# Kernel optimization log

Measured on AMD Instinct MI355X. Metric: run time of the kernel, lower is better.

## Reference

```python
import jax, jax.numpy as jnp
import numpy as np

VOCAB, D, A, NEG = 32000, 200, 20, 2
NUM_USERS, NUM_ITEMS = 100000, 50000
R, L, B, NNZ = 4096, 128, 1024, 20480
EPS = 1e-12

def _norm(x, axis):
    n = jnp.sqrt(jnp.sum(x * x, axis=axis, keepdims=True))
    return x / jnp.maximum(n, EPS)

def setup_inputs() -> dict:
    key = jax.random.key(0)
    ks = jax.random.split(key, 20)
    rows_u = jax.random.randint(ks[5], (NNZ,), 0, B)
    cols_u = jax.random.randint(ks[6], (NNZ,), 0, R)
    rows_i = jax.random.randint(ks[7], (NNZ,), 0, B)
    cols_i = jax.random.randint(ks[8], (NNZ,), 0, R)
    return {
        "historical_review": jax.random.randint(ks[0], (R, L), 0, VOCAB),
        "neg_review": jax.random.randint(ks[1], (R * NEG, L), 0, VOCAB),
        "user": jax.random.randint(ks[2], (B,), 0, NUM_USERS),
        "item": jax.random.randint(ks[3], (B,), 0, NUM_ITEMS),
        "label": jax.random.uniform(ks[4], (B,), jnp.float32, 1.0, 5.0),
        "user_histor_index": jnp.stack([rows_u, cols_u]),
        "user_histor_value": jax.random.uniform(ks[9], (NNZ,), jnp.float32),
        "item_histor_index": jnp.stack([rows_i, cols_i]),
        "item_histor_value": jax.random.uniform(ks[10], (NNZ,), jnp.float32),
        "word_emb": jax.random.normal(ks[11], (VOCAB, D), jnp.float32),
        "Wm": jax.random.normal(ks[12], (D, D), jnp.float32) * 0.05,
        "Ww": jax.random.normal(ks[13], (A, D), jnp.float32) * 0.05,
        "bw": jnp.zeros((A,), jnp.float32),
        "Wt": jax.random.normal(ks[14], (D, A), jnp.float32) * 0.05,
        "fc_w": jax.random.uniform(ks[15], (1, 2 * D), jnp.float32, -0.05, 0.05),
        "fc_b": jnp.zeros((1,), jnp.float32),
        "fm_V": jax.random.uniform(ks[16], (2 * D, 10), jnp.float32, -0.05, 0.05),
        "b_users": jax.random.uniform(ks[17], (NUM_USERS, 1), jnp.float32, 0.0, 0.1),
        "b_items": jax.random.uniform(ks[18], (NUM_ITEMS, 1), jnp.float32, 0.0, 0.1),
    }

def reference(historical_review, neg_review, user, item, label,
              user_histor_index, user_histor_value,
              item_histor_index, item_histor_value,
              word_emb, Wm, Ww, bw, Wt, fc_w, fc_b, fm_V, b_users, b_items):
    # ABAE attention over each review
    e_w = word_emb[historical_review]              # (R, L, D)
    y_s = jnp.mean(e_w, axis=1)                    # (R, D)
    z_n = jnp.mean(word_emb[neg_review], axis=1)   # (R*NEG, D)
    dx = jnp.einsum('rld,rd->rl', e_w @ Wm.T, y_s) # (R, L)
    ax = jax.nn.softmax(dx, axis=1)
    # Faithful to source: view(R, D, L) is a raw reshape, not a transpose.
    z_s = jnp.einsum('rdl,rl->rd', e_w.reshape(R, D, L), ax)  # (R, D)
    p_t = z_s @ Ww.T + bw                          # (R, A)
    r_s = p_t @ Wt.T                               # (R, D)
    # cosine margin ranking loss
    c1 = jnp.sum(_norm(r_s, 1) * _norm(z_s, 1), axis=-1)      # (R,)
    c1 = jnp.repeat(c1, NEG)                                   # (R*NEG,)
    c2 = jnp.sum(_norm(z_n.reshape(R, NEG, D), 2) * _norm(r_s, 1)[:, None, :], axis=-1).reshape(-1)
    abae_out_loss = jax.nn.relu(c2 - c1 + 1.0)     # margin=1, target=+1
    J_loss = jnp.mean(abae_out_loss)
    # aspect-matrix orthogonality regularizer
    Tn = _norm(Wt, 0)                              # normalize columns (dim=0)
    U_loss = jnp.mean((Tn.T @ Tn - jnp.eye(A, dtype=Wt.dtype)) ** 2)
    # sparse (B, R) @ (R, D) aggregation via segment_sum
    user_aspect_embed = jax.ops.segment_sum(
        user_histor_value[:, None] * r_s[user_histor_index[1]],
        user_histor_index[0], num_segments=B)      # (B, D)
    item_aspect_embed = jax.ops.segment_sum(
        item_histor_value[:, None] * r_s[item_histor_index[1]],
        item_histor_index[0], num_segments=B)      # (B, D)
    input_vec = jnp.concatenate([user_aspect_embed, item_aspect_embed], axis=1)  # (B, 2D)
    fm_linear = input_vec @ fc_w.T + fc_b          # (B, 1)
    fm_i1 = (input_vec @ fm_V) ** 2
    fm_i2 = (input_vec ** 2) @ (fm_V ** 2)
    # NOTE: faithful to source, the quadratic term is summed over the whole batch (scalar)
    fm_output = 0.5 * jnp.sum(fm_i1 - fm_i2) + fm_linear + b_users[user] + b_items[item]
    prediction = fm_output.squeeze(1)              # (B,)
    rating_loss = (prediction - label) ** 2
    mse_loss = jnp.mean(rating_loss)
    obj_loss = mse_loss + 0.01 * J_loss + 0.01 * U_loss
    return (obj_loss, rating_loss, abae_out_loss, prediction, user_aspect_embed, item_aspect_embed)
```

## Files before the change

kernel.cpp:

```cpp
#include <hip/hip_runtime.h>
#include <hip/hip_fp16.h>
#include <math.h>

#define R_TOT 4096
#define L_LEN 128
#define D_DIM 200
#define A_DIM 20
#define NEGK  2
#define B_SZ  1024
#define NNZ_C 20480
#define RN_TOT (R_TOT*NEGK)
#define S_TOT (R_TOT + RN_TOT)
#define VOCAB_C 32000
#define EPS_ 1e-12f
#define SLOT_CAP 64
#define NBUCK_BLK 160

__device__ __forceinline__ float4 unpack4(const uint2 u) {
  union { unsigned v; __half2 h; } c0, c1;
  c0.v = u.x; c1.v = u.y;
  const float2 f0 = __half22float2(c0.h);
  const float2 f1 = __half22float2(c1.h);
  return make_float4(f0.x, f0.y, f1.x, f1.y);
}

__global__ __launch_bounds__(256) void k_cast(
    const float* __restrict__ emb, ushort* __restrict__ emb_h, int* __restrict__ cnt)
{
  if (blockIdx.x == 0) {
    for (int i = threadIdx.x; i < 2*B_SZ; i += 256) cnt[i] = 0;
  }
  const int idx = blockIdx.x*256 + threadIdx.x;
  if (idx < (VOCAB_C*D_DIM)/4) {
    const float4 v = reinterpret_cast<const float4*>(emb)[idx];
    ushort4 o;
    o.x = __half_as_ushort(__float2half(v.x));
    o.y = __half_as_ushort(__float2half(v.y));
    o.z = __half_as_ushort(__float2half(v.z));
    o.w = __half_as_ushort(__float2half(v.w));
    reinterpret_cast<ushort4*>(emb_h)[idx] = o;
  }
}

#define ACC8(Q) { \
  const float4 e0_ = unpack4(make_uint2((Q).x,(Q).y)); \
  const float4 e1_ = unpack4(make_uint2((Q).z,(Q).w)); \
  sA.x+=e0_.x; sA.y+=e0_.y; sA.z+=e0_.z; sA.w+=e0_.w; \
  sB.x+=e1_.x; sB.y+=e1_.y; sB.z+=e1_.z; sB.w+=e1_.w; }

__global__ __launch_bounds__(256, 8) void k_means2(
    const int* __restrict__ hist, const int* __restrict__ neg,
    const ushort* __restrict__ emb_h,
    float* __restrict__ ys_all, float* __restrict__ zn_all,
    const int* __restrict__ uidx, const float* __restrict__ uval,
    const int* __restrict__ iidx, const float* __restrict__ ival,
    int* __restrict__ cnt, int* __restrict__ scol, float* __restrict__ sval)
{
  const int sb = blockIdx.x;
  const int tid = threadIdx.x;

  if (sb >= S_TOT) {
    const int g = (sb - S_TOT)*256 + tid;
    if (g < NNZ_C) {
      const int b = uidx[g];
      const int slot = atomicAdd(&cnt[b], 1);
      if (slot < SLOT_CAP) {
        scol[b*SLOT_CAP + slot] = uidx[NNZ_C + g];
        sval[b*SLOT_CAP + slot] = uval[g];
      }
    } else {
      const int g2 = g - NNZ_C;
      const int b = iidx[g2];
      const int slot = atomicAdd(&cnt[B_SZ + b], 1);
      if (slot < SLOT_CAP) {
        scol[(B_SZ + b)*SLOT_CAP + slot] = iidx[NNZ_C + g2];
        sval[(B_SZ + b)*SLOT_CAP + slot] = ival[g2];
      }
    }
    return;
  }

  __shared__ int widx[L_LEN];
  __shared__ __align__(16) float part[8][D_DIM];
  const bool is_pos = (sb < R_TOT);
  const int* src = is_pos ? (hist + (size_t)sb*L_LEN)
                          : (neg + (size_t)(sb - R_TOT)*L_LEN);
  if (tid < L_LEN) widx[tid] = src[tid];
  __syncthreads();

  const int c5 = tid & 31;
  const int j  = tid >> 5;
  float4 sA = {0.f,0.f,0.f,0.f}, sB = {0.f,0.f,0.f,0.f};
  if (c5 < 25) {
    const size_t coff = 8*c5;
    uint4 q0 = *reinterpret_cast<const uint4*>(emb_h + (size_t)widx[j +   0]*D_DIM + coff);
    uint4 q1 = *reinterpret_cast<const uint4*>(emb_h + (size_t)widx[j +   8]*D_DIM + coff);
    uint4 q2 = *reinterpret_cast<const uint4*>(emb_h + (size_t)widx[j +  16]*D_DIM + coff);
    uint4 q3 = *reinterpret_cast<const uint4*>(emb_h + (size_t)widx[j +  24]*D_DIM + coff);
    uint4 q4 = *reinterpret_cast<const uint4*>(emb_h + (size_t)widx[j +  32]*D_DIM + coff);
    uint4 q5 = *reinterpret_cast<const uint4*>(emb_h + (size_t)widx[j +  40]*D_DIM + coff);
    uint4 q6 = *reinterpret_cast<const uint4*>(emb_h + (size_t)widx[j +  48]*D_DIM + coff);
    uint4 q7 = *reinterpret_cast<const uint4*>(emb_h + (size_t)widx[j +  56]*D_DIM + coff);
    ACC8(q0) ACC8(q1) ACC8(q2) ACC8(q3) ACC8(q4) ACC8(q5) ACC8(q6) ACC8(q7)
    q0 = *reinterpret_cast<const uint4*>(emb_h + (size_t)widx[j +  64]*D_DIM + coff);
    q1 = *reinterpret_cast<const uint4*>(emb_h + (size_t)widx[j +  72]*D_DIM + coff);
    q2 = *reinterpret_cast<const uint4*>(emb_h + (size_t)widx[j +  80]*D_DIM + coff);
    q3 = *reinterpret_cast<const uint4*>(emb_h + (size_t)widx[j +  88]*D_DIM + coff);
    q4 = *reinterpret_cast<const uint4*>(emb_h + (size_t)widx[j +  96]*D_DIM + coff);
    q5 = *reinterpret_cast<const uint4*>(emb_h + (size_t)widx[j + 104]*D_DIM + coff);
    q6 = *reinterpret_cast<const uint4*>(emb_h + (size_t)widx[j + 112]*D_DIM + coff);
    q7 = *reinterpret_cast<const uint4*>(emb_h + (size_t)widx[j + 120]*D_DIM + coff);
    ACC8(q0) ACC8(q1) ACC8(q2) ACC8(q3) ACC8(q4) ACC8(q5) ACC8(q6) ACC8(q7)
    *reinterpret_cast<float4*>(&part[j][8*c5])     = sA;
    *reinterpret_cast<float4*>(&part[j][8*c5 + 4]) = sB;
  }
  __syncthreads();
  float* dst = is_pos ? (ys_all + (size_t)sb*D_DIM)
                      : (zn_all + (size_t)(sb - R_TOT)*D_DIM);
  if (tid < D_DIM) {
    float a = 0.f;
    #pragma unroll
    for (int j2 = 0; j2 < 8; ++j2) a += part[j2][tid];
    dst[tid] = a * (1.0f/128.0f);
  }
}

#define KB_RT 16
__global__ __launch_bounds__(256, 2) void k_matvec(
    const float* __restrict__ ys_all, const float* __restrict__ Wm,
    float* __restrict__ vv_all)
{
  __shared__ float ysl[KB_RT][D_DIM];
  const int r0 = blockIdx.x * KB_RT;
  const int tid = threadIdx.x;
  for (int i = tid; i < KB_RT*D_DIM; i += 256)
    ysl[i / D_DIM][i % D_DIM] = ys_all[(size_t)r0*D_DIM + i];
  __syncthreads();
  if (tid < D_DIM) {
    float acc[KB_RT];
    #pragma unroll
    for (int r = 0; r < KB_RT; ++r) acc[r] = 0.f;
    #pragma unroll 4
    for (int k = 0; k < D_DIM; ++k) {
      const float w = Wm[k*D_DIM + tid];
      #pragma unroll
      for (int r = 0; r < KB_RT; ++r) acc[r] += ysl[r][k] * w;
    }
    #pragma unroll
    for (int r = 0; r < KB_RT; ++r)
      vv_all[(size_t)(r0 + r)*D_DIM + tid] = acc[r];
  }
}

__global__ __launch_bounds__(512, 4) void k_attn(
    const int* __restrict__ hist, const ushort* __restrict__ emb_h,
    const float* __restrict__ vv_all,
    const float* __restrict__ Ww, const float* __restrict__ bw,
    const float* __restrict__ Wt, const float* __restrict__ zn_all,
    float* __restrict__ rs_out, float* __restrict__ abae)
{
  __shared__ __align__(16) ushort ew[L_LEN*D_DIM];
  __shared__ __align__(16) float ax[L_LEN];
  __shared__ __align__(16) float zs[D_DIM];
  __shared__ __align__(16) float ubuf[240];
  int*   widx  = reinterpret_cast<int*>(ubuf);
  float* ptile = ubuf;
  float* red   = ubuf + 160;

  const int r = blockIdx.x;
  const int tid = threadIdx.x, lane = tid & 63, wv = tid >> 6;
  const int c5 = tid & 31;
  const int j  = tid >> 5;
  const bool act = (c5 < 25);
  const int coff = 8*c5;

  if (tid < L_LEN) widx[tid] = hist[r*L_LEN + tid];
  float4 v8a = {0,0,0,0}, v8b = {0,0,0,0};
  if (act) {
    v8a = *reinterpret_cast<const float4*>(vv_all + (size_t)r*D_DIM + coff);
    v8b = *reinterpret_cast<const float4*>(vv_all + (size_t)r*D_DIM + coff + 4);
  }
  __syncthreads();

  float zn0 = 0.f, zn1 = 0.f;
  float p0=0.f,p1=0.f,p2=0.f,p3=0.f,p4=0.f,p5=0.f,p6=0.f,p7=0.f;
  {
    uint4 q0,q1,q2,q3,q4,q5,q6,q7;
    if (act) {
      q0 = *reinterpret_cast<const uint4*>(emb_h + (size_t)widx[j +   0]*D_DIM + coff);
      q1 = *reinterpret_cast<const uint4*>(emb_h + (size_t)widx[j +  16]*D_DIM + coff);
      q2 = *reinterpret_cast<const uint4*>(emb_h + (size_t)widx[j +  32]*D_DIM + coff);
      q3 = *reinterpret_cast<const uint4*>(emb_h + (size_t)widx[j +  48]*D_DIM + coff);
      q4 = *reinterpret_cast<const uint4*>(emb_h + (size_t)widx[j +  64]*D_DIM + coff);
      q5 = *reinterpret_cast<const uint4*>(emb_h + (size_t)widx[j +  80]*D_DIM + coff);
      q6 = *reinterpret_cast<const uint4*>(emb_h + (size_t)widx[j +  96]*D_DIM + coff);
      q7 = *reinterpret_cast<const uint4*>(emb_h + (size_t)widx[j + 112]*D_DIM + coff);
    }
    if (tid < D_DIM) {
      zn0 = zn_all[(size_t)(2*r)*D_DIM + tid];
      zn1 = zn_all[(size_t)(2*r + 1)*D_DIM + tid];
    }
    if (act) {
      #define STG(K, Q, P) { \
        *reinterpret_cast<uint4*>(ew + (j + 16*(K))*D_DIM + coff) = Q; \
        const float4 e0_ = unpack4(make_uint2(Q.x, Q.y)); \
        const float4 e1_ = unpack4(make_uint2(Q.z, Q.w)); \
        P = e0_.x*v8a.x + e0_.y*v8a.y + e0_.z*v8a.z + e0_.w*v8a.w \
          + e1_.x*v8b.x + e1_.y*v8b.y + e1_.z*v8b.z + e1_.w*v8b.w; }
      STG(0,q0,p0) STG(1,q1,p1) STG(2,q2,p2) STG(3,q3,p3)
      STG(4,q4,p4) STG(5,q5,p5) STG(6,q6,p6) STG(7,q7,p7)
      #undef STG
    }
  }
  #pragma unroll
  for (int o = 16; o > 0; o >>= 1) {
    p0 += __shfl_xor(p0, o); p1 += __shfl_xor(p1, o);
    p2 += __shfl_xor(p2, o); p3 += __shfl_xor(p3, o);
    p4 += __shfl_xor(p4, o); p5 += __shfl_xor(p5, o);
    p6 += __shfl_xor(p6, o); p7 += __shfl_xor(p7, o);
  }
  if (c5 == 0) {
    ax[j]      = p0; ax[j + 16]  = p1; ax[j + 32]  = p2; ax[j + 48]  = p3;
    ax[j + 64] = p4; ax[j + 80]  = p5; ax[j + 96]  = p6; ax[j + 112] = p7;
  }
  __syncthreads();

  if (tid < 64) {
    float m = fmaxf(ax[tid], ax[tid+64]);
    #pragma unroll
    for (int o = 32; o > 0; o >>= 1) m = fmaxf(m, __shfl_xor(m, o));
    if (tid == 0) red[0] = m;
  }
  __syncthreads();
  const float M = red[0];
  if (tid < L_LEN) {
    float e = expf(ax[tid] - M);
    ax[tid] = e;
    float s = e;
    #pragma unroll
    for (int o = 32; o > 0; o >>= 1) s += __shfl_xor(s, o);
    if (lane == 0) red[1 + wv] = s;
  }
  __syncthreads();

  {
    const float Sinv = 1.0f / (red[1] + red[2]);
    const int lq = lane & 15;
    const int quad = lane >> 4;
    const float4 ax8a = *reinterpret_cast<const float4*>(ax + 8*lq);
    const float4 ax8b = *reinterpret_cast<const float4*>(ax + 8*lq + 4);
    for (int dq = wv; dq < 50; dq += 8) {
      const int d0 = 4*dq + quad;
      const int f0 = (d0 << 7) + 8*lq;
      const uint4 q = *reinterpret_cast<const uint4*>(ew + f0);
      const float4 e0 = unpack4(make_uint2(q.x, q.y));
      const float4 e1 = unpack4(make_uint2(q.z, q.w));
      float a = e0.x*ax8a.x + e0.y*ax8a.y + e0.z*ax8a.z + e0.w*ax8a.w
              + e1.x*ax8b.x + e1.y*ax8b.y + e1.z*ax8b.z + e1.w*ax8b.w;
      #pragma unroll
      for (int o = 8; o > 0; o >>= 1) a += __shfl_xor(a, o);
      if (lq == 0) zs[d0] = a * Sinv;
    }
  }
  __syncthreads();

  if (tid < 160) {
    const int a = tid % 20, jj = tid / 20;
    float s = 0.f;
    #pragma unroll
    for (int ii = 0; ii < 25; ++ii) {
      const int d = jj + 8*ii;
      s += zs[d] * Ww[a*D_DIM + d];
    }
    ptile[tid] = s;
  }
  __syncthreads();
  if (tid < A_DIM) {
    float s = bw[tid];
    #pragma unroll
    for (int jj = 0; jj < 8; ++jj) s += ptile[jj*20 + tid];
    red[2 + tid] = s;
  }
  __syncthreads();

  float rsd = 0.f, zsd = 0.f;
  if (tid < D_DIM) {
    float acc = 0.f;
    #pragma unroll
    for (int a = 0; a < A_DIM; ++a) acc += red[2+a] * Wt[tid*A_DIM + a];
    rsd = acc; zsd = zs[tid];
    rs_out[(size_t)r*D_DIM + tid] = acc;
  } else { zn0 = 0.f; zn1 = 0.f; }
  float a0 = rsd*rsd, a1 = zsd*zsd, a2 = rsd*zsd;
  float b0 = zn0*zn0, b1 = zn0*rsd, b2 = zn1*zn1, b3 = zn1*rsd;
  #pragma unroll
  for (int o = 32; o > 0; o >>= 1) {
    a0 += __shfl_xor(a0, o); a1 += __shfl_xor(a1, o); a2 += __shfl_xor(a2, o);
    b0 += __shfl_xor(b0, o); b1 += __shfl_xor(b1, o);
    b2 += __shfl_xor(b2, o); b3 += __shfl_xor(b3, o);
  }
  if (lane == 0) {
    red[22 + 0*8 + wv] = a0; red[22 + 1*8 + wv] = a1; red[22 + 2*8 + wv] = a2;
    red[22 + 3*8 + wv] = b0; red[22 + 4*8 + wv] = b1;
    red[22 + 5*8 + wv] = b2; red[22 + 6*8 + wv] = b3;
  }
  __syncthreads();

  if (tid < 64) {
    const int qi = tid >> 3, k = tid & 7;
    float v = (qi < 7) ? red[22 + 8*qi + k] : 0.f;
    v += __shfl_xor(v, 1); v += __shfl_xor(v, 2); v += __shfl_xor(v, 4);
    const float s0 = __shfl(v, 0),  s1 = __shfl(v, 8),  s2 = __shfl(v, 16);
    const float t0 = __shfl(v, 24), t1 = __shfl(v, 32);
    const float t2 = __shfl(v, 40), t3 = __shfl(v, 48);
    if (tid == 0) {
      const float nr = fmaxf(sqrtf(s0), EPS_);
      const float nz = fmaxf(sqrtf(s1), EPS_);
      const float c1 = s2 / (nr * nz);
      const float c2a = t1 / (fmaxf(sqrtf(t0), EPS_) * nr);
      const float c2b = t3 / (fmaxf(sqrtf(t2), EPS_) * nr);
      abae[2*r]     = fmaxf(c2a - c1 + 1.0f, 0.0f);
      abae[2*r + 1] = fmaxf(c2b - c1 + 1.0f, 0.0f);
    }
  }
}

__global__ __launch_bounds__(512) void k_aggfm(
    const int* __restrict__ cnt, const int* __restrict__ scol,
    const float* __restrict__ sval, const float* __restrict__ rs,
    const float* __restrict__ fcw, const float* __restrict__ V,
    float* __restrict__ uae, float* __restrict__ iae,
    float* __restrict__ linb, float* __restrict__ quadb)
{
  __shared__ __align__(16) float ivec[2*D_DIM];
  __shared__ float redw[8];
  __shared__ float qpart[10];
  const int b = blockIdx.x;
  const int tid = threadIdx.x, lane = tid & 63, wv = tid >> 6;

  if (tid < D_DIM) {
    int n = cnt[b]; n = n < SLOT_CAP ? n : SLOT_CAP;
    const int* cols = scol + (size_t)b*SLOT_CAP;
    const float* vals = sval + (size_t)b*SLOT_CAP;
    float acc = 0.f;
    for (int j = 0; j < n; ++j) acc += vals[j] * rs[(size_t)cols[j]*D_DIM + tid];
    ivec[tid] = acc;
    uae[(size_t)b*D_DIM + tid] = acc;
  } else if (tid >= 256 && tid < 256 + D_DIM) {
    const int t = tid - 256;
    int n = cnt[B_SZ + b]; n = n < SLOT_CAP ? n : SLOT_CAP;
    const int* cols = scol + (size_t)(B_SZ + b)*SLOT_CAP;
    const float* vals = sval + (size_t)(B_SZ + b)*SLOT_CAP;
    float acc = 0.f;
    for (int j = 0; j < n; ++j) acc += vals[j] * rs[(size_t)cols[j]*D_DIM + t];
    ivec[D_DIM + t] = acc;
    iae[(size_t)b*D_DIM + t] = acc;
  }
  __syncthreads();

  float lv = 0.f;
  if (tid < 2*D_DIM) lv = ivec[tid] * fcw[tid];
  #pragma unroll
  for (int o = 32; o > 0; o >>= 1) lv += __shfl_xor(lv, o);
  if (lane == 0) redw[wv] = lv;

  {
    const int k = wv;
    float s1 = 0.f, s2 = 0.f;
    for (int f = lane; f < 2*D_DIM; f += 64) {
      const float x = ivec[f];
      const float vk = V[f*10 + k];
      s1 += x*vk; s2 += x*x*vk*vk;
    }
    #pragma unroll
    for (int o = 32; o > 0; o >>= 1) { s1 += __shfl_xor(s1,o); s2 += __shfl_xor(s2,o); }
    if (lane == 0) qpart[k] = s1*s1 - s2;
  }
  if (wv < 2) {
    const int k = 8 + wv;
    float s1 = 0.f, s2 = 0.f;
    for (int f = lane; f < 2*D_DIM; f += 64) {
      const float x = ivec[f];
      const float vk = V[f*10 + k];
      s1 += x*vk; s2 += x*x*vk*vk;
    }
    #pragma unroll
    for (int o = 32; o > 0; o >>= 1) { s1 += __shfl_xor(s1,o); s2 += __shfl_xor(s2,o); }
    if (lane == 0) qpart[k] = s1*s1 - s2;
  }
  __syncthreads();
  if (tid == 0) {
    float lin = 0.f;
    #pragma unroll
    for (int i = 0; i < 8; ++i) lin += redw[i];
    float q = 0.f;
    #pragma unroll
    for (int i = 0; i < 10; ++i) q += qpart[i];
    linb[b] = lin; quadb[b] = q;
  }
}

__global__ __launch_bounds__(1024) void k_final2(
    const float* __restrict__ quadb, const float* __restrict__ linb,
    const float* __restrict__ fcb, const int* __restrict__ user,
    const int* __restrict__ item, const float* __restrict__ busers,
    const float* __restrict__ bitems, const float* __restrict__ label,
    const float* __restrict__ Wt, const float* __restrict__ abae,
    float* __restrict__ pred, float* __restrict__ rl, float* __restrict__ obj)
{
  __shared__ float sA[16], sB[16], sC[16];
  __shared__ float cninv[A_DIM];
  __shared__ float quad_s;
  const int tid = threadIdx.x;
  const int lane = tid & 63;
  const int wv = tid >> 6;

  float q = quadb[tid];
  #pragma unroll
  for (int o = 32; o > 0; o >>= 1) q += __shfl_xor(q, o);
  if (lane == 0) sA[wv] = q;

  if (tid < A_DIM) {
    float s = 0.f;
    for (int d = 0; d < D_DIM; ++d) { const float w = Wt[d*A_DIM + tid]; s += w*w; }
    cninv[tid] = 1.0f / fmaxf(sqrtf(s), EPS_);
  }
  __syncthreads();
  if (wv == 0) {
    float s = (lane < 16) ? sA[lane] : 0.f;
    #pragma unroll
    for (int o = 32; o > 0; o >>= 1) s += __shfl_xor(s, o);
    if (lane == 0) quad_s = s;
  }
  __syncthreads();

  const float p = 0.5f*quad_s + linb[tid] + fcb[0]
                + busers[user[tid]] + bitems[item[tid]];
  pred[tid] = p;
  const float dd = p - label[tid];
  const float myrl = dd*dd;
  rl[tid] = myrl;

  float u = 0.f;
  if (tid < 400) {
    const int a = tid / 20, c = tid % 20;
    float dot = 0.f;
    for (int d = 0; d < D_DIM; ++d) dot += Wt[d*A_DIM + a]*Wt[d*A_DIM + c];
    const float g = dot*cninv[a]*cninv[c] - (a==c ? 1.0f : 0.0f);
    u = g*g;
  }
  float js = 0.f;
  #pragma unroll
  for (int j = 0; j < 8; ++j) js += abae[tid + 1024*j];
  float ms = myrl;

  #pragma unroll
  for (int o = 32; o > 0; o >>= 1) {
    u += __shfl_xor(u,o); js += __shfl_xor(js,o); ms += __shfl_xor(ms,o);
  }
  if (lane == 0) { sA[wv] = u; sB[wv] = js; sC[wv] = ms; }
  __syncthreads();
  if (tid == 0) {
    float U = 0.f, J = 0.f, Ms = 0.f;
    for (int i = 0; i < 16; ++i) { U += sA[i]; J += sB[i]; Ms += sC[i]; }
    obj[0] = Ms/1024.0f + 0.01f*(J/8192.0f) + 0.01f*(U/400.0f);
  }
}

extern "C" void kernel_launch(void* const* d_in, const int* in_sizes, int n_in,
                              void* d_out, int out_size, void* d_ws, size_t ws_size,
                              hipStream_t stream) {
  const int*   hist   = (const int*)  d_in[0];
  const int*   neg    = (const int*)  d_in[1];
  const int*   user   = (const int*)  d_in[2];
  const int*   item   = (const int*)  d_in[3];
  const float* label  = (const float*)d_in[4];
  const int*   uidx   = (const int*)  d_in[5];
  const float* uval   = (const float*)d_in[6];
  const int*   iidx   = (const int*)  d_in[7];
  const float* ival   = (const float*)d_in[8];
  const float* emb    = (const float*)d_in[9];
  const float* Wm     = (const float*)d_in[10];
  const float* Ww     = (const float*)d_in[11];
  const float* bw     = (const float*)d_in[12];
  const float* Wt     = (const float*)d_in[13];
  const float* fcw    = (const float*)d_in[14];
  const float* fcb    = (const float*)d_in[15];
  const float* V      = (const float*)d_in[16];
  const float* busers = (const float*)d_in[17];
  const float* bitems = (const float*)d_in[18];

  float* out  = (float*)d_out;
  float* obj  = out;
  float* rl   = out + 1;
  float* abae = out + 1 + B_SZ;
  float* pred = out + 1 + B_SZ + RN_TOT;
  float* uae  = pred + B_SZ;
  float* iae  = uae + (size_t)B_SZ*D_DIM;

  float* ws     = (float*)d_ws;
  float* rs     = ws;
  float* ys_all = rs + (size_t)R_TOT*D_DIM;
  float* zn_all = ys_all + (size_t)R_TOT*D_DIM;
  float* vv_all = zn_all + (size_t)RN_TOT*D_DIM;
  float* linb   = vv_all + (size_t)R_TOT*D_DIM;
  float* quadb  = linb + B_SZ;
  float* sval   = quadb + B_SZ;
  int*   scol   = (int*)(sval + (size_t)2*B_SZ*SLOT_CAP);
  int*   cnt    = scol + (size_t)2*B_SZ*SLOT_CAP;
  ushort* emb_h = (ushort*)(cnt + 2*B_SZ);

  const int cast_blocks = (VOCAB_C*D_DIM/4 + 255)/256;

  k_cast  <<<cast_blocks, 256, 0, stream>>>(emb, emb_h, cnt);
  k_means2<<<S_TOT + NBUCK_BLK, 256, 0, stream>>>(hist, neg, emb_h,
                                                  ys_all, zn_all,
                                                  uidx, uval, iidx, ival,
                                                  cnt, scol, sval);
  k_matvec<<<R_TOT/KB_RT, 256, 0, stream>>>(ys_all, Wm, vv_all);
  k_attn  <<<R_TOT, 512, 0, stream>>>(hist, emb_h, vv_all, Ww, bw, Wt,
                                      zn_all, rs, abae);
  k_aggfm <<<B_SZ, 512, 0, stream>>>(cnt, scol, sval, rs, fcw, V,
                                     uae, iae, linb, quadb);
  k_final2<<<1, 1024, 0, stream>>>(quadb, linb, fcb, user, item, busers, bitems,
                                   label, Wt, abae, pred, rl, obj);
}
```

Measured before the change: 309.2 us.

## Keep gathered embeddings in registers, reduce with DPP, raise attn occupancy

```diff
diff --git a/kernel.cpp b/kernel.cpp
--- a/kernel.cpp
+++ b/kernel.cpp
@@ -22,6 +22,39 @@
   const float2 f0 = __half22float2(c0.h);
   const float2 f1 = __half22float2(c1.h);
   return make_float4(f0.x, f0.y, f1.x, f1.y);
+}
+
+__device__ __forceinline__ float dot8h(const uint4 q, const float4 va, const float4 vb) {
+  const float4 e0 = unpack4(make_uint2(q.x, q.y));
+  const float4 e1 = unpack4(make_uint2(q.z, q.w));
+  return e0.x*va.x + e0.y*va.y + e0.z*va.z + e0.w*va.w
+       + e1.x*vb.x + e1.y*vb.y + e1.z*vb.z + e1.w*vb.w;
+}
+
+#define DPPI(old_, src_, ctrl, rmask) \
+  __builtin_amdgcn_update_dpp(old_, src_, ctrl, rmask, 0xf, false)
+
+__device__ __forceinline__ float dpp_sum32(float s) {
+  s += __int_as_float(DPPI(0, __float_as_int(s), 0x111, 0xf));
+  s += __int_as_float(DPPI(0, __float_as_int(s), 0x112, 0xf));
+  s += __int_as_float(DPPI(0, __float_as_int(s), 0x114, 0xf));
+  s += __int_as_float(DPPI(0, __float_as_int(s), 0x118, 0xf));
+  s += __int_as_float(DPPI(0, __float_as_int(s), 0x142, 0xa));
+  return s;
+}
+__device__ __forceinline__ float dpp_sum64(float s) {
+  s = dpp_sum32(s);
+  s += __int_as_float(DPPI(0, __float_as_int(s), 0x143, 0xc));
+  return s;
+}
+__device__ __forceinline__ float dpp_max64(float s) {
+  s = fmaxf(s, __int_as_float(DPPI(__float_as_int(s), __float_as_int(s), 0x111, 0xf)));
+  s = fmaxf(s, __int_as_float(DPPI(__float_as_int(s), __float_as_int(s), 0x112, 0xf)));
+  s = fmaxf(s, __int_as_float(DPPI(__float_as_int(s), __float_as_int(s), 0x114, 0xf)));
+  s = fmaxf(s, __int_as_float(DPPI(__float_as_int(s), __float_as_int(s), 0x118, 0xf)));
+  s = fmaxf(s, __int_as_float(DPPI(__float_as_int(s), __float_as_int(s), 0x142, 0xa)));
+  s = fmaxf(s, __int_as_float(DPPI(__float_as_int(s), __float_as_int(s), 0x143, 0xc)));
+  return s;
 }
 
 __global__ __launch_bounds__(256) void k_cast(
@@ -152,14 +185,14 @@
   }
 }
 
-__global__ __launch_bounds__(512, 4) void k_attn(
+__global__ __launch_bounds__(512, 6) void k_attn(
     const int* __restrict__ hist, const ushort* __restrict__ emb_h,
     const float* __restrict__ vv_all,
     const float* __restrict__ Ww, const float* __restrict__ bw,
     const float* __restrict__ Wt, const float* __restrict__ zn_all,
     float* __restrict__ rs_out, float* __restrict__ abae)
 {
-  __shared__ __align__(16) ushort ew[L_LEN*D_DIM];
+  __shared__ __align__(16) float part[D_DIM][16];
   __shared__ __align__(16) float ax[L_LEN];
   __shared__ __align__(16) float zs[D_DIM];
   __shared__ __align__(16) float ubuf[240];
@@ -182,85 +215,79 @@
   }
   __syncthreads();
 
+  uint4 q0,q1,q2,q3,q4,q5,q6,q7;
+  q0=q1=q2=q3=q4=q5=q6=q7=make_uint4(0,0,0,0);
   float zn0 = 0.f, zn1 = 0.f;
   float p0=0.f,p1=0.f,p2=0.f,p3=0.f,p4=0.f,p5=0.f,p6=0.f,p7=0.f;
-  {
-    uint4 q0,q1,q2,q3,q4,q5,q6,q7;
-    if (act) {
-      q0 = *reinterpret_cast<const uint4*>(emb_h + (size_t)widx[j +   0]*D_DIM + coff);
-      q1 = *reinterpret_cast<const uint4*>(emb_h + (size_t)widx[j +  16]*D_DIM + coff);
-      q2 = *reinterpret_cast<const uint4*>(emb_h + (size_t)widx[j +  32]*D_DIM + coff);
-      q3 = *reinterpret_cast<const uint4*>(emb_h + (size_t)widx[j +  48]*D_DIM + coff);
-      q4 = *reinterpret_cast<const uint4*>(emb_h + (size_t)widx[j +  64]*D_DIM + coff);
-      q5 = *reinterpret_cast<const uint4*>(emb_h + (size_t)widx[j +  80]*D_DIM + coff);
-      q6 = *reinterpret_cast<const uint4*>(emb_h + (size_t)widx[j +  96]*D_DIM + coff);
-      q7 = *reinterpret_cast<const uint4*>(emb_h + (size_t)widx[j + 112]*D_DIM + coff);
-    }
-    if (tid < D_DIM) {
-      zn0 = zn_all[(size_t)(2*r)*D_DIM + tid];
-      zn1 = zn_all[(size_t)(2*r + 1)*D_DIM + tid];
-    }
-    if (act) {
-      #define STG(K, Q, P) { \
-        *reinterpret_cast<uint4*>(ew + (j + 16*(K))*D_DIM + coff) = Q; \
-        const float4 e0_ = unpack4(make_uint2(Q.x, Q.y)); \
-        const float4 e1_ = unpack4(make_uint2(Q.z, Q.w)); \
-        P = e0_.x*v8a.x + e0_.y*v8a.y + e0_.z*v8a.z + e0_.w*v8a.w \
-          + e1_.x*v8b.x + e1_.y*v8b.y + e1_.z*v8b.z + e1_.w*v8b.w; }
-      STG(0,q0,p0) STG(1,q1,p1) STG(2,q2,p2) STG(3,q3,p3)
-      STG(4,q4,p4) STG(5,q5,p5) STG(6,q6,p6) STG(7,q7,p7)
-      #undef STG
-    }
-  }
-  #pragma unroll
-  for (int o = 16; o > 0; o >>= 1) {
-    p0 += __shfl_xor(p0, o); p1 += __shfl_xor(p1, o);
-    p2 += __shfl_xor(p2, o); p3 += __shfl_xor(p3, o);
-    p4 += __shfl_xor(p4, o); p5 += __shfl_xor(p5, o);
-    p6 += __shfl_xor(p6, o); p7 += __shfl_xor(p7, o);
-  }
-  if (c5 == 0) {
+  if (act) {
+    q0 = *reinterpret_cast<const uint4*>(emb_h + (size_t)widx[j +   0]*D_DIM + coff);
+    q1 = *reinterpret_cast<const uint4*>(emb_h + (size_t)widx[j +  16]*D_DIM + coff);
+    q2 = *reinterpret_cast<const uint4*>(emb_h + (size_t)widx[j +  32]*D_DIM + coff);
+    q3 = *reinterpret_cast<const uint4*>(emb_h + (size_t)widx[j +  48]*D_DIM + coff);
+    q4 = *reinterpret_cast<const uint4*>(emb_h + (size_t)widx[j +  64]*D_DIM + coff);
+    q5 = *reinterpret_cast<const uint4*>(emb_h + (size_t)widx[j +  80]*D_DIM + coff);
+    q6 = *reinterpret_cast<const uint4*>(emb_h + (size_t)widx[j +  96]*D_DIM + coff);
+    q7 = *reinterpret_cast<const uint4*>(emb_h + (size_t)widx[j + 112]*D_DIM + coff);
+  }
+  if (tid < D_DIM) {
+    zn0 = zn_all[(size_t)(2*r)*D_DIM + tid];
+    zn1 = zn_all[(size_t)(2*r + 1)*D_DIM + tid];
+  }
+  if (act) {
+    p0 = dot8h(q0, v8a, v8b); p1 = dot8h(q1, v8a, v8b);
+    p2 = dot8h(q2, v8a, v8b); p3 = dot8h(q3, v8a, v8b);
+    p4 = dot8h(q4, v8a, v8b); p5 = dot8h(q5, v8a, v8b);
+    p6 = dot8h(q6, v8a, v8b); p7 = dot8h(q7, v8a, v8b);
+  }
+  p0 = dpp_sum32(p0); p1 = dpp_sum32(p1); p2 = dpp_sum32(p2); p3 = dpp_sum32(p3);
+  p4 = dpp_sum32(p4); p5 = dpp_sum32(p5); p6 = dpp_sum32(p6); p7 = dpp_sum32(p7);
+  if (c5 == 31) {
     ax[j]      = p0; ax[j + 16]  = p1; ax[j + 32]  = p2; ax[j + 48]  = p3;
     ax[j + 64] = p4; ax[j + 80]  = p5; ax[j + 96]  = p6; ax[j + 112] = p7;
   }
   __syncthreads();
 
   if (tid < 64) {
-    float m = fmaxf(ax[tid], ax[tid+64]);
-    #pragma unroll
-    for (int o = 32; o > 0; o >>= 1) m = fmaxf(m, __shfl_xor(m, o));
-    if (tid == 0) red[0] = m;
+    float m = dpp_max64(fmaxf(ax[tid], ax[tid+64]));
+    if (tid == 63) red[0] = m;
   }
   __syncthreads();
   const float M = red[0];
   if (tid < L_LEN) {
-    float e = expf(ax[tid] - M);
+    const float e = expf(ax[tid] - M);
     ax[tid] = e;
-    float s = e;
-    #pragma unroll
-    for (int o = 32; o > 0; o >>= 1) s += __shfl_xor(s, o);
-    if (lane == 0) red[1 + wv] = s;
-  }
-  __syncthreads();
-
-  {
+    const float s = dpp_sum64(e);
+    if (lane == 63) red[1 + wv] = s;
+  }
+  __syncthreads();
+
+  if (act) {
+    const int Y  = 25*j + c5;
+    const int l0 = (8*Y) & 127;
+    const int v0 = Y >> 4;
+    const int sl = Y & 15;
+    const float4 ax8a = *reinterpret_cast<const float4*>(ax + l0);
+    const float4 ax8b = *reinterpret_cast<const float4*>(ax + l0 + 4);
+    part[v0 +   0][sl] = dot8h(q0, ax8a, ax8b);
+    part[v0 +  25][sl] = dot8h(q1, ax8a, ax8b);
+    part[v0 +  50][sl] = dot8h(q2, ax8a, ax8b);
+    part[v0 +  75][sl] = dot8h(q3, ax8a, ax8b);
+    part[v0 + 100][sl] = dot8h(q4, ax8a, ax8b);
+    part[v0 + 125][sl] = dot8h(q5, ax8a, ax8b);
+    part[v0 + 150][sl] = dot8h(q6, ax8a, ax8b);
+    part[v0 + 175][sl] = dot8h(q7, ax8a, ax8b);
+  }
+  __syncthreads();
+
+  if (tid < D_DIM) {
     const float Sinv = 1.0f / (red[1] + red[2]);
-    const int lq = lane & 15;
-    const int quad = lane >> 4;
-    const float4 ax8a = *reinterpret_cast<const float4*>(ax + 8*lq);
-    const float4 ax8b = *reinterpret_cast<const float4*>(ax + 8*lq + 4);
-    for (int dq = wv; dq < 50; dq += 8) {
-      const int d0 = 4*dq + quad;
-      const int f0 = (d0 << 7) + 8*lq;
-      const uint4 q = *reinterpret_cast<const uint4*>(ew + f0);
-      const float4 e0 = unpack4(make_uint2(q.x, q.y));
-      const float4 e1 = unpack4(make_uint2(q.z, q.w));
-      float a = e0.x*ax8a.x + e0.y*ax8a.y + e0.z*ax8a.z + e0.w*ax8a.w
-              + e1.x*ax8b.x + e1.y*ax8b.y + e1.z*ax8b.z + e1.w*ax8b.w;
-      #pragma unroll
-      for (int o = 8; o > 0; o >>= 1) a += __shfl_xor(a, o);
-      if (lq == 0) zs[d0] = a * Sinv;
-    }
+    const float4 a0 = *reinterpret_cast<const float4*>(&part[tid][0]);
+    const float4 a1 = *reinterpret_cast<const float4*>(&part[tid][4]);
+    const float4 a2 = *reinterpret_cast<const float4*>(&part[tid][8]);
+    const float4 a3 = *reinterpret_cast<const float4*>(&part[tid][12]);
+    const float s = ((a0.x+a0.y)+(a0.z+a0.w)) + ((a1.x+a1.y)+(a1.z+a1.w))
+                  + ((a2.x+a2.y)+(a2.z+a2.w)) + ((a3.x+a3.y)+(a3.z+a3.w));
+    zs[tid] = s * Sinv;
   }
   __syncthreads();
 
@@ -291,15 +318,10 @@
     rsd = acc; zsd = zs[tid];
     rs_out[(size_t)r*D_DIM + tid] = acc;
   } else { zn0 = 0.f; zn1 = 0.f; }
-  float a0 = rsd*rsd, a1 = zsd*zsd, a2 = rsd*zsd;
-  float b0 = zn0*zn0, b1 = zn0*rsd, b2 = zn1*zn1, b3 = zn1*rsd;
-  #pragma unroll
-  for (int o = 32; o > 0; o >>= 1) {
-    a0 += __shfl_xor(a0, o); a1 += __shfl_xor(a1, o); a2 += __shfl_xor(a2, o);
-    b0 += __shfl_xor(b0, o); b1 += __shfl_xor(b1, o);
-    b2 += __shfl_xor(b2, o); b3 += __shfl_xor(b3, o);
-  }
-  if (lane == 0) {
+  float a0 = dpp_sum64(rsd*rsd), a1 = dpp_sum64(zsd*zsd), a2 = dpp_sum64(rsd*zsd);
+  float b0 = dpp_sum64(zn0*zn0), b1 = dpp_sum64(zn0*rsd);
+  float b2 = dpp_sum64(zn1*zn1), b3 = dpp_sum64(zn1*rsd);
+  if (lane == 63) {
     red[22 + 0*8 + wv] = a0; red[22 + 1*8 + wv] = a1; red[22 + 2*8 + wv] = a2;
     red[22 + 3*8 + wv] = b0; red[22 + 4*8 + wv] = b1;
     red[22 + 5*8 + wv] = b2; red[22 + 6*8 + wv] = b3;
```

Measured after the change: 297.1 us. 3.9% less time.
